# Optimization experiments

Hardware: AMD Instinct MI355X
Metric: run time of the kernel (lower is better)

Reference implementation:

```python
import jax, jax.numpy as jnp
import numpy as np

B, N_HEADS, DIM = 8, 12, 768
T0, H0, W0 = 8, 14, 14
HEAD_DIM = DIM // N_HEADS  # 64
SCALE = HEAD_DIM ** -0.5
EPS = 1e-5


def setup_inputs() -> dict:
    key = jax.random.key(0)
    ks = jax.random.split(key, 10)
    N = T0 * H0 * W0
    def g(k, shape, sc=0.02):
        return jax.random.normal(k, shape, jnp.float32) * sc
    return {
        "x": jax.random.normal(ks[0], (B, N, DIM), jnp.float32),
        "w_qkv": g(ks[1], (DIM, 3 * DIM)),
        "b_qkv": jnp.zeros((3 * DIM,), jnp.float32),
        "pool_q_w": g(ks[2], (HEAD_DIM, 1, 3, 3, 3), 0.1),
        "pool_k_w": g(ks[3], (HEAD_DIM, 1, 3, 3, 3), 0.1),
        "pool_v_w": g(ks[4], (HEAD_DIM, 1, 3, 3, 3), 0.1),
        "norm_q_g": jnp.ones((HEAD_DIM,), jnp.float32),
        "norm_q_b": jnp.zeros((HEAD_DIM,), jnp.float32),
        "norm_k_g": jnp.ones((HEAD_DIM,), jnp.float32),
        "norm_k_b": jnp.zeros((HEAD_DIM,), jnp.float32),
        "norm_v_g": jnp.ones((HEAD_DIM,), jnp.float32),
        "norm_v_b": jnp.zeros((HEAD_DIM,), jnp.float32),
        "rel_pos_h": g(ks[5], (26, HEAD_DIM)),  # max dist idx 25 for q_h=14,k_h=7
        "rel_pos_w": g(ks[6], (26, HEAD_DIM)),
        "rel_pos_t": g(ks[7], (15, HEAD_DIM)),  # 2*8-1
        "w_proj": g(ks[8], (DIM, DIM)),
        "b_proj": jnp.zeros((DIM,), jnp.float32),
        "t": T0, "h": H0, "w": W0,
    }


def _layer_norm(x, g, b):
    m = jnp.mean(x, -1, keepdims=True)
    v = jnp.mean(jnp.square(x - m), -1, keepdims=True)
    return (x - m) * jax.lax.rsqrt(v + EPS) * g + b


def _attn_pool(x, wk, g, b, thw, stride):
    # x: [B, heads, L, C]; depthwise conv3d pooling + LayerNorm(head_dim)
    Bb, nh, L, C = x.shape
    t, h, w = thw
    y = x.reshape(Bb * nh, t, h, w, C).transpose(0, 4, 1, 2, 3)  # [B*nh, C, t, h, w]
    y = jax.lax.conv_general_dilated(
        y, wk, stride, [(1, 1), (1, 1), (1, 1)],
        dimension_numbers=("NCDHW", "OIDHW", "NCDHW"),
        feature_group_count=C)
    thw2 = tuple(y.shape[2:])
    y = y.reshape(Bb, nh, C, -1).transpose(0, 1, 3, 2)  # [B, nh, L', C]
    return _layer_norm(y, g, b), thw2


def _rel_dist(qn, kn):
    q_ratio = max(kn / qn, 1.0)
    k_ratio = max(qn / kn, 1.0)
    d = (np.arange(qn)[:, None] * q_ratio
         - np.arange(kn)[None, :] * k_ratio
         + (kn - 1) * k_ratio)
    return d.astype(np.int64)


def _rel_bias(q, q_shape, k_shape, Rh, Rw, Rt):
    qt, qh, qw = q_shape
    kt, kh, kw = k_shape
    Bb, nh, _, C = q.shape
    r_q = q.reshape(Bb, nh, qt, qh, qw, C)
    rel_h = jnp.einsum('bythwc,hkc->bythwk', r_q, Rh[_rel_dist(qh, kh)])
    rel_w = jnp.einsum('bythwc,wkc->bythwk', r_q, Rw[_rel_dist(qw, kw)])
    rel_t = jnp.einsum('bythwc,tkc->bythwk', r_q, Rt[_rel_dist(qt, kt)])
    bias = (rel_h[:, :, :, :, :, None, :, None]
            + rel_w[:, :, :, :, :, None, None, :]
            + rel_t[:, :, :, :, :, :, None, None])  # [B,nh,qt,qh,qw,kt,kh,kw]
    return bias.reshape(Bb, nh, qt * qh * qw, kt * kh * kw)


def reference(x, w_qkv, b_qkv, pool_q_w, pool_k_w, pool_v_w,
              norm_q_g, norm_q_b, norm_k_g, norm_k_b, norm_v_g, norm_v_b,
              rel_pos_h, rel_pos_w, rel_pos_t, w_proj, b_proj, t, h, w):
    Bb, N, _ = x.shape
    qkv = (x @ w_qkv + b_qkv).reshape(Bb, N, 3, N_HEADS, HEAD_DIM).transpose(2, 0, 3, 1, 4)
    q, k, v = qkv[0], qkv[1], qkv[2]  # each [B, nh, N, head_dim]
    q, q_shape = _attn_pool(q, pool_q_w, norm_q_g, norm_q_b, (t, h, w), (1, 1, 1))
    k, k_shape = _attn_pool(k, pool_k_w, norm_k_g, norm_k_b, (t, h, w), (1, 2, 2))
    v, _ = _attn_pool(v, pool_v_w, norm_v_g, norm_v_b, (t, h, w), (1, 2, 2))
    attn = jnp.einsum('bhqc,bhkc->bhqk', q * SCALE, k)
    attn = attn + _rel_bias(q, q_shape, k_shape, rel_pos_h, rel_pos_w, rel_pos_t)
    attn = jax.nn.softmax(attn, axis=-1)
    out = jnp.einsum('bhqk,bhkc->bhqc', attn, v)
    out = out.transpose(0, 2, 1, 3).reshape(Bb, -1, DIM)
    return out @ w_proj + b_proj
```

## Files before the change

### kernel.cpp

```cpp
#include <hip/hip_runtime.h>
#include <hip/hip_bf16.h>

#define BATCH 8
#define NH 12
#define DIM 768
#define HD 64
#define NQ 1568
#define TT 8
#define HH_ 14
#define WW_ 14
#define LK 392
#define LKP 416
#define SCALE 0.125f
#define EPS 1e-5f

#define QKVS ((size_t)BATCH * NH * NQ * HD)

typedef __bf16 bf16x8 __attribute__((ext_vector_type(8)));
typedef float f32x4 __attribute__((ext_vector_type(4)));

__device__ inline ushort f2bf(float f) {
  __bf16 h = (__bf16)f;
  return __builtin_bit_cast(ushort, h);
}
__device__ inline float bf2f(ushort v) { return __uint_as_float((uint)v << 16); }
__device__ inline float bfl(uint u) { return __uint_as_float(u << 16); }
__device__ inline float bfh(uint u) { return __uint_as_float(u & 0xffff0000u); }

__device__ inline void gload_lds16(const ushort* g, ushort* l) {
  __builtin_amdgcn_global_load_lds(
      (const __attribute__((address_space(1))) void*)g,
      (__attribute__((address_space(3))) void*)l, 16, 0, 0);
}

__global__ __launch_bounds__(256) void zero_kernel(uint4* __restrict__ p, int n16) {
  int i = blockIdx.x * 256 + threadIdx.x;
  int stride = gridDim.x * 256;
  for (; i < n16; i += stride) p[i] = make_uint4(0, 0, 0, 0);
}

__global__ __launch_bounds__(256) void cast_bf16(const float* __restrict__ in,
                                                 ushort* __restrict__ outb, int n) {
  int i = (blockIdx.x * blockDim.x + threadIdx.x) * 4;
  if (i >= n) return;
  float4 v = *(const float4*)(in + i);
  ushort4 o = make_ushort4(f2bf(v.x), f2bf(v.y), f2bf(v.z), f2bf(v.w));
  *(ushort4*)(outb + i) = o;
}

__global__ __launch_bounds__(256) void transpose_cast(const float* __restrict__ in,
                                                      ushort* __restrict__ outb,
                                                      int R, int C) {
  __shared__ float tile[32][33];
  int tx = threadIdx.x & 31, ty = threadIdx.x >> 5;
  int bx = blockIdx.x * 32;
  int by = blockIdx.y * 32;
#pragma unroll
  for (int r = 0; r < 4; ++r)
    tile[ty + r * 8][tx] = in[(size_t)(by + ty + r * 8) * C + bx + tx];
  __syncthreads();
#pragma unroll
  for (int r = 0; r < 4; ++r)
    outb[(size_t)(bx + ty + r * 8) * R + by + tx] = f2bf(tile[tx][ty + r * 8]);
}

__global__ __launch_bounds__(256) void wpool_transpose(const float* __restrict__ wq,
                                                       const float* __restrict__ wk,
                                                       const float* __restrict__ wv,
                                                       float* __restrict__ wT) {
  int i = blockIdx.x * blockDim.x + threadIdx.x;
  if (i >= 3 * 27 * 64) return;
  int s = i / (27 * 64), r = i % (27 * 64), tap = r / 64, c = r % 64;
  const float* src = (s == 0) ? wq : ((s == 1) ? wk : wv);
  wT[i] = src[c * 27 + tap];
}

template<int EPI>
__global__ __launch_bounds__(256) void gemm_mfma(const ushort* __restrict__ A,
                                                 const ushort* __restrict__ Bt,
                                                 const float* __restrict__ bias,
                                                 float* __restrict__ outf,
                                                 ushort* __restrict__ outp,
                                                 int M, int N, int K) {
  __shared__ ushort As[128 * 32];
  __shared__ ushort Bs[128 * 32];
  const int tid = threadIdx.x;
  const int wave = tid >> 6, lane = tid & 63;
  const int quad = lane >> 4, l16 = lane & 15;
  const int row0 = blockIdx.y * 128;
  const int col0 = blockIdx.x * 128;
  const int wm = (wave & 1) * 64;
  const int wn = (wave >> 1) * 64;

  f32x4 acc[4][4];
#pragma unroll
  for (int i = 0; i < 4; ++i)
#pragma unroll
    for (int j = 0; j < 4; ++j) acc[i][j] = (f32x4){0.f, 0.f, 0.f, 0.f};

  const int srow = (wave << 4) + (lane >> 2);
  const int scol = (lane & 3) << 3;
  ushort* ldsA = As + wave * 512;
  ushort* ldsB = Bs + wave * 512;
  const ushort* gA = A + (size_t)(row0 + srow) * K + scol;
  const ushort* gB = Bt + (size_t)(col0 + srow) * K + scol;

  for (int k0 = 0; k0 < K; k0 += 32) {
    __syncthreads();
    gload_lds16(gA + k0, ldsA);
    gload_lds16(gA + (size_t)64 * K + k0, ldsA + 2048);
    gload_lds16(gB + k0, ldsB);
    gload_lds16(gB + (size_t)64 * K + k0, ldsB + 2048);
    __syncthreads();
    bf16x8 af[4], bfr[4];
#pragma unroll
    for (int i = 0; i < 4; ++i)
      af[i] = *(const bf16x8*)&As[(wm + i * 16 + l16) * 32 + quad * 8];
#pragma unroll
    for (int j = 0; j < 4; ++j)
      bfr[j] = *(const bf16x8*)&Bs[(wn + j * 16 + l16) * 32 + quad * 8];
#pragma unroll
    for (int i = 0; i < 4; ++i)
#pragma unroll
      for (int j = 0; j < 4; ++j)
        acc[i][j] = __builtin_amdgcn_mfma_f32_16x16x32_bf16(af[i], bfr[j], acc[i][j], 0, 0, 0);
  }

#pragma unroll
  for (int i = 0; i < 4; ++i) {
#pragma unroll
    for (int j = 0; j < 4; ++j) {
      int col = col0 + wn + j * 16 + l16;
      float bv = bias[col];
#pragma unroll
      for (int r = 0; r < 4; ++r) {
        int row = row0 + wm + i * 16 + quad * 4 + r;
        float val = acc[i][j][r] + bv;
        if (EPI == 0) {
          outf[(size_t)row * N + col] = val;
        } else {
          int b = row / NQ, nn = row % NQ;
          int s = col / DIM, rr = col % DIM;
          int h = rr >> 6, cc = rr & 63;
          size_t pidx = (((size_t)s * BATCH * NH + b * NH + h) * NQ + nn) * (size_t)HD + cc;
          outp[pidx] = f2bf(val);
        }
      }
    }
  }
}

template<int SW, int OWW, int VT>
__global__ __launch_bounds__(256) void pool_ln_row(const ushort* __restrict__ in,
                                                   ushort* __restrict__ out,
                                                   const float* __restrict__ wT,
                                                   const float* __restrict__ g,
                                                   const float* __restrict__ bb) {
  const int OH = OWW;
  const int wid = (blockIdx.x * blockDim.x + threadIdx.x) >> 6;
  const int lane = threadIdx.x & 63;
  const int rowsTot = BATCH * NH * TT * OH;
  if (wid >= rowsTot) return;
  const int bh = wid / (TT * OH);
  const int rr = wid % (TT * OH);
  const int ot = rr / OH, oy = rr % OH;
  const int c = lane;

  float wv[27];
#pragma unroll
  for (int i = 0; i < 27; ++i) wv[i] = wT[i * 64 + c];

  float acc[OWW];
#pragma unroll
  for (int o = 0; o < OWW; ++o) acc[o] = 0.f;

  const ushort* bhbase = in + (size_t)bh * NQ * HD + c;
#pragma unroll
  for (int dt = 0; dt < 3; ++dt) {
    int tt = ot + dt - 1;
    if (tt < 0 || tt >= TT) continue;
#pragma unroll
    for (int dy = 0; dy < 3; ++dy) {
      int yy = oy * SW + dy - 1;
      if (yy < 0 || yy >= HH_) continue;
      const ushort* rowb = bhbase + (size_t)(tt * (HH_ * WW_) + yy * WW_) * HD;
      const float* wrow = &wv[(dt * 3 + dy) * 3];
#pragma unroll
      for (int xx = 0; xx < WW_; ++xx) {
        float v = bf2f(rowb[(size_t)xx * HD]);
#pragma unroll
        for (int dx = 0; dx < 3; ++dx) {
          int num = xx + 1 - dx;
          if (SW == 1) {
            if (num >= 0 && num < OWW) acc[num] += v * wrow[dx];
          } else {
            if (num >= 0 && (num & 1) == 0 && (num >> 1) < OWW)
              acc[num >> 1] += v * wrow[dx];
          }
        }
      }
    }
  }

#pragma unroll
  for (int o = 0; o < OWW; ++o) {
    float a = acc[o];
    float s = a;
#pragma unroll
    for (int off = 32; off; off >>= 1) s += __shfl_xor(s, off, 64);
    float mean = s * (1.f / 64.f);
    float d = a - mean;
    float vs = d * d;
#pragma unroll
    for (int off = 32; off; off >>= 1) vs += __shfl_xor(vs, off, 64);
    float inv = rsqrtf(vs * (1.f / 64.f) + EPS);
    float res = d * inv * g[c] + bb[c];
    int opos = (ot * OH + oy) * OWW + o;
    if (VT == 0) out[((size_t)bh * (TT * OH * OWW) + opos) * HD + c] = f2bf(res);
    else         out[((size_t)bh * HD + c) * LKP + opos] = f2bf(res);
  }
}

__global__ __launch_bounds__(256) void rel_gemm(const ushort* __restrict__ qp,
                                                const float* __restrict__ Rh,
                                                const float* __restrict__ Rw,
                                                const float* __restrict__ Rt,
                                                float* __restrict__ rel) {
  __shared__ ushort sR[80 * 72];
  const int tid = threadIdx.x;
  const int wave = tid >> 6, lane = tid & 63;
  const int quad = lane >> 4, l16 = lane & 15;
  const int row0 = blockIdx.x * 128;

  for (int e = tid; e < 80 * 64; e += 256) {
    int n = e >> 6, k = e & 63;
    float v;
    if (n < 26)      v = Rh[n * 64 + k];
    else if (n < 52) v = Rw[(n - 26) * 64 + k];
    else if (n < 67) v = Rt[(n - 52) * 64 + k];
    else             v = 0.f;
    sR[n * 72 + k] = f2bf(v);
  }
  __syncthreads();

  const int rbase = row0 + wave * 32;
  bf16x8 af[2][2];
#pragma unroll
  for (int m = 0; m < 2; ++m)
#pragma unroll
    for (int ks = 0; ks < 2; ++ks)
      af[m][ks] = *(const bf16x8*)(qp + (size_t)(rbase + m * 16 + l16) * HD + ks * 32 + quad * 8);

  f32x4 acc[2][5];
#pragma unroll
  for (int m = 0; m < 2; ++m)
#pragma unroll
    for (int n = 0; n < 5; ++n) acc[m][n] = (f32x4){0.f, 0.f, 0.f, 0.f};

#pragma unroll
  for (int n = 0; n < 5; ++n) {
#pragma unroll
    for (int ks = 0; ks < 2; ++ks) {
      bf16x8 bfr = *(const bf16x8*)&sR[(n * 16 + l16) * 72 + ks * 32 + quad * 8];
#pragma unroll
      for (int m = 0; m < 2; ++m)
        acc[m][n] = __builtin_amdgcn_mfma_f32_16x16x32_bf16(af[m][ks], bfr, acc[m][n], 0, 0, 0);
    }
  }

#pragma unroll
  for (int m = 0; m < 2; ++m) {
#pragma unroll
    for (int r = 0; r < 4; ++r) {
      int q = rbase + m * 16 + quad * 4 + r;
      int n_ = q % NQ;
      int t = n_ / 196, r2 = n_ % 196, y = r2 / 14, x = r2 % 14;
      float* relq = rel + (size_t)q * 24;
#pragma unroll
      for (int n = 0; n < 5; ++n) {
        int c = n * 16 + l16;
        float val = acc[m][n][r];
        if (c < 26) {
          int dy = y + 12 - c;
          if (dy >= 0 && dy <= 12 && (dy & 1) == 0) relq[dy >> 1] = val;
        } else if (c < 52) {
          int dx = x + 12 - (c - 26);
          if (dx >= 0 && dx <= 12 && (dx & 1) == 0) relq[7 + (dx >> 1)] = val;
        } else if (c < 67) {
          int dt = t + 7 - (c - 52);
          if (dt >= 0 && dt <= 7) relq[14 + dt] = val;
        }
      }
    }
  }
}

__global__ __launch_bounds__(256) void attn_mfma(const ushort* __restrict__ qp,
                                                 const ushort* __restrict__ kp,
                                                 const ushort* __restrict__ vT,
                                                 const float* __restrict__ rel,
                                                 ushort* __restrict__ outb) {
  __shared__ ushort sP[32][424];
  __shared__ float sRelT[24][36];
  __shared__ float sMax[32][4];
  __shared__ float sSum[32][4];
  const int qb = blockIdx.x;
  const int bh = blockIdx.y;
  const int b = bh / NH, h = bh % NH;
  const int tid = threadIdx.x;
  const int w = tid >> 6, lane = tid & 63;
  const int quad = lane >> 4, l16 = lane & 15;
  const int q0 = qb * 32;

  const ushort* qbase = qp + ((size_t)bh * NQ + q0) * HD;
  bf16x8 af[2][2];
#pragma unroll
  for (int t = 0; t < 2; ++t) {
    af[t][0] = *(const bf16x8*)(qbase + (size_t)(t * 16 + l16) * HD + quad * 8);
    af[t][1] = *(const bf16x8*)(qbase + (size_t)(t * 16 + l16) * HD + 32 + quad * 8);
  }

  const float* relbase = rel + ((size_t)bh * NQ + q0) * 24;
  for (int e = tid; e < 32 * 22; e += 256) {
    int row = e / 22, j = e % 22;
    sRelT[j][row] = relbase[row * 24 + j];
  }
  if (tid < 64) {
    int row = tid >> 1, seg = tid & 1;
    *(uint4*)&sP[row][400 + seg * 8] = make_uint4(0, 0, 0, 0);
  }

  f32x4 acc[7][2];
#pragma unroll
  for (int c = 0; c < 7; ++c)
#pragma unroll
    for (int t = 0; t < 2; ++t) acc[c][t] = (f32x4){0.f, 0.f, 0.f, 0.f};

  const ushort* kbase = kp + (size_t)bh * LK * HD;
#pragma unroll
  for (int c = 0; c < 7; ++c) {
    int tg = c * 4 + w;
    if (tg < 25) {
      int kg = tg * 16 + l16;
      int kgc = kg < LK ? kg : (LK - 1);
      const ushort* krow = kbase + (size_t)kgc * HD;
      bf16x8 b0 = *(const bf16x8*)(krow + quad * 8);
      bf16x8 b1 = *(const bf16x8*)(krow + 32 + quad * 8);
#pragma unroll
      for (int t = 0; t < 2; ++t) {
        acc[c][t] = __builtin_amdgcn_mfma_f32_16x16x32_bf16(af[t][0], b0, acc[c][t], 0, 0, 0);
        acc[c][t] = __builtin_amdgcn_mfma_f32_16x16x32_bf16(af[t][1], b1, acc[c][t], 0, 0, 0);
      }
    }
  }
  __syncthreads();

#pragma unroll
  for (int c = 0; c < 7; ++c) {
    int tg = c * 4 + w;
    int kg = tg * 16 + l16;
    if (tg < 25) {
      int kgc = kg < LK ? kg : 0;
      bool ok = kg < LK;
      int kt = kgc / 49, kyx = kgc % 49, ky = kyx / 7, kx = kyx % 7;
#pragma unroll
      for (int t = 0; t < 2; ++t) {
        f32x4 bh4 = *(const f32x4*)&sRelT[ky][t * 16 + quad * 4];
        f32x4 bw4 = *(const f32x4*)&sRelT[7 + kx][t * 16 + quad * 4];
        f32x4 bt4 = *(const f32x4*)&sRelT[14 + kt][t * 16 + quad * 4];
#pragma unroll
        for (int r = 0; r < 4; ++r)
          acc[c][t][r] = ok ? (acc[c][t][r] * SCALE + bh4[r] + bw4[r] + bt4[r]) : -1e30f;
      }
    } else {
#pragma unroll
      for (int t = 0; t < 2; ++t)
#pragma unroll
        for (int r = 0; r < 4; ++r) acc[c][t][r] = -1e30f;
    }
  }

  float pmax[2][4];
#pragma unroll
  for (int t = 0; t < 2; ++t)
#pragma unroll
    for (int r = 0; r < 4; ++r) {
      float m = acc[0][t][r];
#pragma unroll
      for (int c = 1; c < 7; ++c) m = fmaxf(m, acc[c][t][r]);
#pragma unroll
      for (int off = 1; off < 16; off <<= 1) m = fmaxf(m, __shfl_xor(m, off, 64));
      pmax[t][r] = m;
    }
  if (l16 == 0) {
#pragma unroll
    for (int t = 0; t < 2; ++t)
#pragma unroll
      for (int r = 0; r < 4; ++r) sMax[t * 16 + quad * 4 + r][w] = pmax[t][r];
  }
  __syncthreads();

  float M[2][4];
#pragma unroll
  for (int t = 0; t < 2; ++t)
#pragma unroll
    for (int r = 0; r < 4; ++r) {
      float4 mm = *(float4*)&sMax[t * 16 + quad * 4 + r][0];
      M[t][r] = fmaxf(fmaxf(mm.x, mm.y), fmaxf(mm.z, mm.w));
    }

  float psum[2][4];
#pragma unroll
  for (int t = 0; t < 2; ++t)
#pragma unroll
    for (int r = 0; r < 4; ++r) psum[t][r] = 0.f;
#pragma unroll
  for (int c = 0; c < 7; ++c) {
#pragma unroll
    for (int t = 0; t < 2; ++t)
#pragma unroll
      for (int r = 0; r < 4; ++r) {
        float e = __expf(acc[c][t][r] - M[t][r]);
        acc[c][t][r] = e;
        psum[t][r] += e;
      }
  }
#pragma unroll
  for (int t = 0; t < 2; ++t)
#pragma unroll
    for (int r = 0; r < 4; ++r) {
      float s = psum[t][r];
#pragma unroll
      for (int off = 1; off < 16; off <<= 1) s += __shfl_xor(s, off, 64);
      psum[t][r] = s;
    }
  if (l16 == 0) {
#pragma unroll
    for (int t = 0; t < 2; ++t)
#pragma unroll
      for (int r = 0; r < 4; ++r) sSum[t * 16 + quad * 4 + r][w] = psum[t][r];
  }
#pragma unroll
  for (int c = 0; c < 7; ++c) {
    int tg = c * 4 + w;
    if (tg < 25) {
      int kg = tg * 16 + l16;
#pragma unroll
      for (int t = 0; t < 2; ++t)
#pragma unroll
        for (int r = 0; r < 4; ++r)
          sP[t * 16 + quad * 4 + r][kg] = f2bf(acc[c][t][r]);
    }
  }
  __syncthreads();

  float rinv[2][4];
#pragma unroll
  for (int t = 0; t < 2; ++t)
#pragma unroll
    for (int r = 0; r < 4; ++r) {
      float4 ss = *(float4*)&sSum[t * 16 + quad * 4 + r][0];
      rinv[t][r] = 1.f / (ss.x + ss.y + ss.z + ss.w);
    }

  f32x4 oacc[2];
  oacc[0] = (f32x4){0.f, 0.f, 0.f, 0.f};
  oacc[1] = (f32x4){0.f, 0.f, 0.f, 0.f};
  const ushort* vrow = vT + ((size_t)bh * HD + w * 16 + l16) * LKP;
#pragma unroll
  for (int s = 0; s < 13; ++s) {
    int kb = s * 32;
    bf16x8 vb = *(const bf16x8*)(vrow + kb + quad * 8);
#pragma unroll
    for (int t = 0; t < 2; ++t) {
      bf16x8 pa = *(const bf16x8*)&sP[t * 16 + l16][kb + quad * 8];
      oacc[t] = __builtin_amdgcn_mfma_f32_16x16x32_bf16(pa, vb, oacc[t], 0, 0, 0);
    }
  }

#pragma unroll
  for (int t = 0; t < 2; ++t)
#pragma unroll
    for (int r = 0; r < 4; ++r) {
      int q = q0 + t * 16 + quad * 4 + r;
      outb[((size_t)b * NQ + q) * DIM + h * HD + w * 16 + l16] = f2bf(oacc[t][r] * rinv[t][r]);
    }
}

extern "C" void kernel_launch(void* const* d_in, const int* in_sizes, int n_in,
                              void* d_out, int out_size, void* d_ws, size_t ws_size,
                              hipStream_t stream) {
  const float* x        = (const float*)d_in[0];
  const float* w_qkv    = (const float*)d_in[1];
  const float* b_qkv    = (const float*)d_in[2];
  const float* pool_q_w = (const float*)d_in[3];
  const float* pool_k_w = (const float*)d_in[4];
  const float* pool_v_w = (const float*)d_in[5];
  const float* norm_q_g = (const float*)d_in[6];
  const float* norm_q_b = (const float*)d_in[7];
  const float* norm_k_g = (const float*)d_in[8];
  const float* norm_k_b = (const float*)d_in[9];
  const float* norm_v_g = (const float*)d_in[10];
  const float* norm_v_b = (const float*)d_in[11];
  const float* rel_h    = (const float*)d_in[12];
  const float* rel_w    = (const float*)d_in[13];
  const float* rel_t    = (const float*)d_in[14];
  const float* w_proj   = (const float*)d_in[15];
  const float* b_proj   = (const float*)d_in[16];
  float* out = (float*)d_out;

  const size_t NT  = (size_t)BATCH * NH * NQ * HD;
  const size_t LKT = (size_t)BATCH * NH * LK * HD;
  const size_t LKV = (size_t)BATCH * NH * HD * LKP;
  const size_t RELN = (size_t)BATCH * NH * NQ * 24;

  ushort* qkvb = (ushort*)d_ws;
  ushort* qpb  = qkvb + 3 * QKVS;
  ushort* kpb  = qpb + NT;
  ushort* vTb  = kpb + LKT;
  float*  relb = (float*)(vTb + LKV);
  ushort* wqkvT = (ushort*)(relb + RELN);
  ushort* wprojT = wqkvT + (size_t)DIM * 3 * DIM;
  float*  wpoolT = (float*)(wprojT + (size_t)DIM * DIM);
  ushort* xb = qpb;
  ushort* attn_outb = qkvb;

  const int M = BATCH * NQ;

  zero_kernel<<<256, 256, 0, stream>>>((uint4*)vTb, (int)(LKV * 2 / 16));
  {
    int n = M * DIM;
    cast_bf16<<<(n / 4 + 255) / 256, 256, 0, stream>>>(x, xb, n);
    transpose_cast<<<dim3(3 * DIM / 32, DIM / 32), 256, 0, stream>>>(w_qkv, wqkvT, DIM, 3 * DIM);
    transpose_cast<<<dim3(DIM / 32, DIM / 32), 256, 0, stream>>>(w_proj, wprojT, DIM, DIM);
    wpool_transpose<<<(3 * 27 * 64 + 255) / 256, 256, 0, stream>>>(
        pool_q_w, pool_k_w, pool_v_w, wpoolT);
  }

  gemm_mfma<1><<<dim3(3 * DIM / 128, M / 128), 256, 0, stream>>>(
      xb, wqkvT, b_qkv, nullptr, qkvb, M, 3 * DIM, DIM);

  {
    pool_ln_row<1, 14, 0><<<(BATCH * NH * TT * 14) / 4, 256, 0, stream>>>(
        qkvb, qpb, wpoolT, norm_q_g, norm_q_b);
    pool_ln_row<2, 7, 0><<<(BATCH * NH * TT * 7) / 4, 256, 0, stream>>>(
        qkvb + QKVS, kpb, wpoolT + 27 * 64, norm_k_g, norm_k_b);
    pool_ln_row<2, 7, 1><<<(BATCH * NH * TT * 7) / 4, 256, 0, stream>>>(
        qkvb + 2 * QKVS, vTb, wpoolT + 2 * 27 * 64, norm_v_g, norm_v_b);
  }

  rel_gemm<<<(BATCH * NH * NQ) / 128, 256, 0, stream>>>(
      qpb, rel_h, rel_w, rel_t, relb);

  attn_mfma<<<dim3(NQ / 32, BATCH * NH), 256, 0, stream>>>(qpb, kpb, vTb, relb, attn_outb);

  gemm_mfma<0><<<dim3(DIM / 128, M / 128), 256, 0, stream>>>(
      attn_outb, wprojT, b_proj, out, nullptr, M, DIM, DIM);
}
```

Baseline: 427.3 us.

## Fuse prep kernels, double-buffer GEMM LDS loads, fold attention scale into K

Merges the zero, cast, weight-transpose and pool-weight-transpose launches into one prep kernel dispatched by block index, which removes several launch overheads. The MFMA GEMM now keeps two LDS buffers and issues the loads for the next K tile before computing on the current one, aiming to hide global-load latency behind the MFMAs. The 1/sqrt(d) scale is applied to pooled K at normalisation time instead of to every attention score. That removes a multiply per score but changes where the bf16 rounding happens. The single-sync double-buffer scheme relies on how global_load_lds completion is ordered against the barrier.

```diff
diff --git a/kernel.cpp b/kernel.cpp
--- a/kernel.cpp
+++ b/kernel.cpp
@@ -16,6 +16,12 @@
 
 #define QKVS ((size_t)BATCH * NH * NQ * HD)
 
+#define NB_CAST 2048
+#define NB_TQKV 1728
+#define NB_TPROJ 576
+#define NB_ZERO 64
+#define NB_WPOOL 21
+
 typedef __bf16 bf16x8 __attribute__((ext_vector_type(8)));
 typedef float f32x4 __attribute__((ext_vector_type(4)));
 
@@ -24,8 +30,6 @@
   return __builtin_bit_cast(ushort, h);
 }
 __device__ inline float bf2f(ushort v) { return __uint_as_float((uint)v << 16); }
-__device__ inline float bfl(uint u) { return __uint_as_float(u << 16); }
-__device__ inline float bfh(uint u) { return __uint_as_float(u & 0xffff0000u); }
 
 __device__ inline void gload_lds16(const ushort* g, ushort* l) {
   __builtin_amdgcn_global_load_lds(
@@ -33,46 +37,57 @@
       (__attribute__((address_space(3))) void*)l, 16, 0, 0);
 }
 
-__global__ __launch_bounds__(256) void zero_kernel(uint4* __restrict__ p, int n16) {
-  int i = blockIdx.x * 256 + threadIdx.x;
-  int stride = gridDim.x * 256;
-  for (; i < n16; i += stride) p[i] = make_uint4(0, 0, 0, 0);
-}
-
-__global__ __launch_bounds__(256) void cast_bf16(const float* __restrict__ in,
-                                                 ushort* __restrict__ outb, int n) {
-  int i = (blockIdx.x * blockDim.x + threadIdx.x) * 4;
-  if (i >= n) return;
-  float4 v = *(const float4*)(in + i);
-  ushort4 o = make_ushort4(f2bf(v.x), f2bf(v.y), f2bf(v.z), f2bf(v.w));
-  *(ushort4*)(outb + i) = o;
-}
-
-__global__ __launch_bounds__(256) void transpose_cast(const float* __restrict__ in,
-                                                      ushort* __restrict__ outb,
-                                                      int R, int C) {
+__global__ __launch_bounds__(256) void prep_kernel(
+    const float* __restrict__ x, const float* __restrict__ w_qkv,
+    const float* __restrict__ w_proj,
+    const float* __restrict__ wq, const float* __restrict__ wk,
+    const float* __restrict__ wv,
+    ushort* __restrict__ xb, ushort* __restrict__ wqkvT,
+    ushort* __restrict__ wprojT, float* __restrict__ wT,
+    uint4* __restrict__ zp, int nzero16, int ncast4) {
   __shared__ float tile[32][33];
-  int tx = threadIdx.x & 31, ty = threadIdx.x >> 5;
-  int bx = blockIdx.x * 32;
-  int by = blockIdx.y * 32;
-#pragma unroll
-  for (int r = 0; r < 4; ++r)
-    tile[ty + r * 8][tx] = in[(size_t)(by + ty + r * 8) * C + bx + tx];
-  __syncthreads();
-#pragma unroll
-  for (int r = 0; r < 4; ++r)
-    outb[(size_t)(bx + ty + r * 8) * R + by + tx] = f2bf(tile[tx][ty + r * 8]);
-}
-
-__global__ __launch_bounds__(256) void wpool_transpose(const float* __restrict__ wq,
-                                                       const float* __restrict__ wk,
-                                                       const float* __restrict__ wv,
-                                                       float* __restrict__ wT) {
-  int i = blockIdx.x * blockDim.x + threadIdx.x;
-  if (i >= 3 * 27 * 64) return;
-  int s = i / (27 * 64), r = i % (27 * 64), tap = r / 64, c = r % 64;
-  const float* src = (s == 0) ? wq : ((s == 1) ? wk : wv);
-  wT[i] = src[c * 27 + tap];
+  int bid = blockIdx.x;
+  const int tid = threadIdx.x;
+  if (bid < NB_CAST) {
+    for (int i = bid * 256 + tid; i < ncast4; i += NB_CAST * 256) {
+      float4 v = *(const float4*)(x + (size_t)i * 4);
+      *(ushort4*)(xb + (size_t)i * 4) =
+          make_ushort4(f2bf(v.x), f2bf(v.y), f2bf(v.z), f2bf(v.w));
+    }
+    return;
+  }
+  bid -= NB_CAST;
+  if (bid < NB_TQKV + NB_TPROJ) {
+    const float* in; ushort* outb; int R, C, bx, by;
+    if (bid < NB_TQKV) { in = w_qkv; outb = wqkvT; R = DIM; C = 3 * DIM;
+                         bx = (bid % 72) * 32; by = (bid / 72) * 32; }
+    else { int b2 = bid - NB_TQKV; in = w_proj; outb = wprojT; R = DIM; C = DIM;
+           bx = (b2 % 24) * 32; by = (b2 / 24) * 32; }
+    int tx = tid & 31, ty = tid >> 5;
+#pragma unroll
+    for (int r = 0; r < 4; ++r)
+      tile[ty + r * 8][tx] = in[(size_t)(by + ty + r * 8) * C + bx + tx];
+    __syncthreads();
+#pragma unroll
+    for (int r = 0; r < 4; ++r)
+      outb[(size_t)(bx + ty + r * 8) * R + by + tx] = f2bf(tile[tx][ty + r * 8]);
+    return;
+  }
+  bid -= NB_TQKV + NB_TPROJ;
+  if (bid < NB_ZERO) {
+    for (int i = bid * 256 + tid; i < nzero16; i += NB_ZERO * 256)
+      zp[i] = make_uint4(0, 0, 0, 0);
+    return;
+  }
+  bid -= NB_ZERO;
+  {
+    int i = bid * 256 + tid;
+    if (i < 3 * 27 * 64) {
+      int s = i / (27 * 64), r = i % (27 * 64), tap = r / 64, c = r % 64;
+      const float* src = (s == 0) ? wq : ((s == 1) ? wk : wv);
+      wT[i] = src[c * 27 + tap];
+    }
+  }
 }
 
 template<int EPI>
@@ -82,8 +97,8 @@
                                                  float* __restrict__ outf,
                                                  ushort* __restrict__ outp,
                                                  int M, int N, int K) {
-  __shared__ ushort As[128 * 32];
-  __shared__ ushort Bs[128 * 32];
+  __shared__ ushort As[2][128 * 32];
+  __shared__ ushort Bs[2][128 * 32];
   const int tid = threadIdx.x;
   const int wave = tid >> 6, lane = tid & 63;
   const int quad = lane >> 4, l16 = lane & 15;
@@ -100,30 +115,38 @@
 
   const int srow = (wave << 4) + (lane >> 2);
   const int scol = (lane & 3) << 3;
-  ushort* ldsA = As + wave * 512;
-  ushort* ldsB = Bs + wave * 512;
   const ushort* gA = A + (size_t)(row0 + srow) * K + scol;
   const ushort* gB = Bt + (size_t)(col0 + srow) * K + scol;
 
+  gload_lds16(gA, &As[0][wave * 512]);
+  gload_lds16(gA + (size_t)64 * K, &As[0][wave * 512 + 2048]);
+  gload_lds16(gB, &Bs[0][wave * 512]);
+  gload_lds16(gB + (size_t)64 * K, &Bs[0][wave * 512 + 2048]);
+  __syncthreads();
+
+  int cur = 0;
   for (int k0 = 0; k0 < K; k0 += 32) {
-    __syncthreads();
-    gload_lds16(gA + k0, ldsA);
-    gload_lds16(gA + (size_t)64 * K + k0, ldsA + 2048);
-    gload_lds16(gB + k0, ldsB);
-    gload_lds16(gB + (size_t)64 * K + k0, ldsB + 2048);
-    __syncthreads();
+    if (k0 + 32 < K) {
+      int nb = cur ^ 1;
+      gload_lds16(gA + k0 + 32, &As[nb][wave * 512]);
+      gload_lds16(gA + (size_t)64 * K + k0 + 32, &As[nb][wave * 512 + 2048]);
+      gload_lds16(gB + k0 + 32, &Bs[nb][wave * 512]);
+      gload_lds16(gB + (size_t)64 * K + k0 + 32, &Bs[nb][wave * 512 + 2048]);
+    }
     bf16x8 af[4], bfr[4];
 #pragma unroll
     for (int i = 0; i < 4; ++i)
-      af[i] = *(const bf16x8*)&As[(wm + i * 16 + l16) * 32 + quad * 8];
+      af[i] = *(const bf16x8*)&As[cur][(wm + i * 16 + l16) * 32 + quad * 8];
 #pragma unroll
     for (int j = 0; j < 4; ++j)
-      bfr[j] = *(const bf16x8*)&Bs[(wn + j * 16 + l16) * 32 + quad * 8];
+      bfr[j] = *(const bf16x8*)&Bs[cur][(wn + j * 16 + l16) * 32 + quad * 8];
 #pragma unroll
     for (int i = 0; i < 4; ++i)
 #pragma unroll
       for (int j = 0; j < 4; ++j)
         acc[i][j] = __builtin_amdgcn_mfma_f32_16x16x32_bf16(af[i], bfr[j], acc[i][j], 0, 0, 0);
+    __syncthreads();
+    cur ^= 1;
   }
 
 #pragma unroll
@@ -155,7 +178,8 @@
                                                    ushort* __restrict__ out,
                                                    const float* __restrict__ wT,
                                                    const float* __restrict__ g,
-                                                   const float* __restrict__ bb) {
+                                                   const float* __restrict__ bb,
+                                                   float oscale) {
   const int OH = OWW;
   const int wid = (blockIdx.x * blockDim.x + threadIdx.x) >> 6;
   const int lane = threadIdx.x & 63;
@@ -214,7 +238,7 @@
 #pragma unroll
     for (int off = 32; off; off >>= 1) vs += __shfl_xor(vs, off, 64);
     float inv = rsqrtf(vs * (1.f / 64.f) + EPS);
-    float res = d * inv * g[c] + bb[c];
+    float res = (d * inv * g[c] + bb[c]) * oscale;
     int opos = (ot * OH + oy) * OWW + o;
     if (VT == 0) out[((size_t)bh * (TT * OH * OWW) + opos) * HD + c] = f2bf(res);
     else         out[((size_t)bh * HD + c) * LKP + opos] = f2bf(res);
@@ -370,7 +394,7 @@
         f32x4 bt4 = *(const f32x4*)&sRelT[14 + kt][t * 16 + quad * 4];
 #pragma unroll
         for (int r = 0; r < 4; ++r)
-          acc[c][t][r] = ok ? (acc[c][t][r] * SCALE + bh4[r] + bw4[r] + bt4[r]) : -1e30f;
+          acc[c][t][r] = ok ? (acc[c][t][r] + bh4[r] + bw4[r] + bt4[r]) : -1e30f;
       }
     } else {
 #pragma unroll
@@ -527,26 +551,20 @@
 
   const int M = BATCH * NQ;
 
-  zero_kernel<<<256, 256, 0, stream>>>((uint4*)vTb, (int)(LKV * 2 / 16));
-  {
-    int n = M * DIM;
-    cast_bf16<<<(n / 4 + 255) / 256, 256, 0, stream>>>(x, xb, n);
-    transpose_cast<<<dim3(3 * DIM / 32, DIM / 32), 256, 0, stream>>>(w_qkv, wqkvT, DIM, 3 * DIM);
-    transpose_cast<<<dim3(DIM / 32, DIM / 32), 256, 0, stream>>>(w_proj, wprojT, DIM, DIM);
-    wpool_transpose<<<(3 * 27 * 64 + 255) / 256, 256, 0, stream>>>(
-        pool_q_w, pool_k_w, pool_v_w, wpoolT);
-  }
+  prep_kernel<<<NB_CAST + NB_TQKV + NB_TPROJ + NB_ZERO + NB_WPOOL, 256, 0, stream>>>(
+      x, w_qkv, w_proj, pool_q_w, pool_k_w, pool_v_w,
+      xb, wqkvT, wprojT, wpoolT, (uint4*)vTb, (int)(LKV * 2 / 16), M * DIM / 4);
 
   gemm_mfma<1><<<dim3(3 * DIM / 128, M / 128), 256, 0, stream>>>(
       xb, wqkvT, b_qkv, nullptr, qkvb, M, 3 * DIM, DIM);
 
   {
     pool_ln_row<1, 14, 0><<<(BATCH * NH * TT * 14) / 4, 256, 0, stream>>>(
-        qkvb, qpb, wpoolT, norm_q_g, norm_q_b);
+        qkvb, qpb, wpoolT, norm_q_g, norm_q_b, 1.0f);
     pool_ln_row<2, 7, 0><<<(BATCH * NH * TT * 7) / 4, 256, 0, stream>>>(
-        qkvb + QKVS, kpb, wpoolT + 27 * 64, norm_k_g, norm_k_b);
+        qkvb + QKVS, kpb, wpoolT + 27 * 64, norm_k_g, norm_k_b, SCALE);
     pool_ln_row<2, 7, 1><<<(BATCH * NH * TT * 7) / 4, 256, 0, stream>>>(
-        qkvb + 2 * QKVS, vTb, wpoolT + 2 * 27 * 64, norm_v_g, norm_v_b);
+        qkvb + 2 * QKVS, vTb, wpoolT + 2 * 27 * 64, norm_v_g, norm_v_b, 1.0f);
   }
 
   rel_gemm<<<(BATCH * NH * NQ) / 128, 256, 0, stream>>>(
```

After: 409.1 us. -4.2%, faster.
